# Performance work log

Measured on AMD Instinct MI355X. Metric: run time of the kernel, lower is better.

The kernel has to match this reference:

```python
import jax, jax.numpy as jnp
import numpy as np

N_NODES = 100000
N_EDGES = 50000
NNZ = 800000
D_IN = 128
D_OUT = 128


def setup_inputs() -> dict:
    key = jax.random.key(0)
    k1, k2, k3, k4, k5 = jax.random.split(key, 5)
    x_0 = jax.random.normal(k1, (N_NODES, D_IN), dtype=jnp.float32)
    W = jax.random.normal(k2, (D_OUT, D_IN), dtype=jnp.float32) / np.sqrt(D_IN)
    b = jax.random.normal(k3, (D_OUT,), dtype=jnp.float32) * 0.01
    node_ids = jax.random.randint(k4, (NNZ,), 0, N_NODES, dtype=jnp.int32)
    edge_ids = jax.random.randint(k5, (NNZ,), 0, N_EDGES, dtype=jnp.int32)
    return {"x_0": x_0, "W": W, "b": b, "node_ids": node_ids, "edge_ids": edge_ids}


def reference(x_0, W, b, node_ids, edge_ids):
    # Linear transform (no batchnorm: use_bn=False)
    x = x_0 @ W.T + b  # [n_nodes, out_channels]

    # Step 1: hyperedge aggregation (e_aggr='sum'):  m_{0->1} = B_1^T x, reduce=sum
    m01 = jax.ops.segment_sum(x[node_ids], edge_ids, num_segments=N_EDGES)  # [n_edges, d]

    # Step 2: node aggregation (v_aggr='mean'):  m_{1->0} = B_1 m_{0->1}, reduce=mean
    s = jax.ops.segment_sum(m01[edge_ids], node_ids, num_segments=N_NODES)  # [n_nodes, d]
    cnt = jax.ops.segment_sum(jnp.ones((NNZ,), dtype=x.dtype), node_ids, num_segments=N_NODES)
    m10 = s / jnp.maximum(cnt, 1.0)[:, None]

    # Step 3: SAGE update (residual add)
    return x + m10
```

## Files before the change

### kernel.cpp

```cpp
#include <hip/hip_runtime.h>
#include <hip/hip_bf16.h>

#define NN 100000
#define NE 50000
#define NZ 800000
#define D  128
#define NSEG (NE + NN)
#define FILL_P 4
#define FILL_B 782

typedef __bf16 bf16x8 __attribute__((ext_vector_type(8)));
typedef float f32x4 __attribute__((ext_vector_type(4)));

static __device__ __forceinline__ unsigned short f2bf(float f) {
  union { float f; unsigned u; } v; v.f = f;
  unsigned r = (v.u + 0x7FFFu + ((v.u >> 16) & 1u)) >> 16;
  return (unsigned short)r;
}
static __device__ __forceinline__ float bf2f(unsigned short h) {
  union { unsigned u; float f; } v; v.u = ((unsigned)h) << 16;
  return v.f;
}

__global__ __launch_bounds__(256) void unisage_gemm_mfma(const float* __restrict__ x0,
                                                         const float* __restrict__ W,
                                                         const float* __restrict__ bias,
                                                         unsigned short* __restrict__ xb) {
  __shared__ __bf16 Wl[128][136];
  const int t = threadIdx.x;
#pragma unroll
  for (int i = 0; i < 16; ++i) {
    int idx = i * 1024 + t * 4;
    int dout = idx >> 7;
    int k = idx & 127;
    float4 wv = *(const float4*)(W + idx);
    Wl[dout][k + 0] = (__bf16)wv.x;
    Wl[dout][k + 1] = (__bf16)wv.y;
    Wl[dout][k + 2] = (__bf16)wv.z;
    Wl[dout][k + 3] = (__bf16)wv.w;
  }
  __syncthreads();

  const int wave = t >> 6;
  const int lane = t & 63;
  const int lr = lane & 15;
  const int lg = lane >> 4;
  const int rowbase = blockIdx.x * 128 + wave * 32;

  f32x4 acc[2][8] = {};

#pragma unroll
  for (int ks = 0; ks < 4; ++ks) {
    const int k0 = ks * 32 + lg * 8;
    bf16x8 b[8];
#pragma unroll
    for (int cf = 0; cf < 8; ++cf)
      b[cf] = *(const bf16x8*)&Wl[cf * 16 + lr][k0];
#pragma unroll
    for (int rf = 0; rf < 2; ++rf) {
      int row = rowbase + rf * 16 + lr;
      row = row < NN ? row : NN - 1;
      const float* src = x0 + (size_t)row * D + k0;
      float4 f0 = *(const float4*)(src);
      float4 f1 = *(const float4*)(src + 4);
      bf16x8 a;
      a[0] = (__bf16)f0.x; a[1] = (__bf16)f0.y;
      a[2] = (__bf16)f0.z; a[3] = (__bf16)f0.w;
      a[4] = (__bf16)f1.x; a[5] = (__bf16)f1.y;
      a[6] = (__bf16)f1.z; a[7] = (__bf16)f1.w;
#pragma unroll
      for (int cf = 0; cf < 8; ++cf)
        acc[rf][cf] = __builtin_amdgcn_mfma_f32_16x16x32_bf16(a, b[cf], acc[rf][cf], 0, 0, 0);
    }
  }

#pragma unroll
  for (int cf = 0; cf < 8; ++cf) {
    float bv = bias[cf * 16 + lr];
#pragma unroll
    for (int rf = 0; rf < 2; ++rf) {
#pragma unroll
      for (int r = 0; r < 4; ++r) {
        int row = rowbase + rf * 16 + lg * 4 + r;
        if (row < NN)
          xb[(size_t)row * D + cf * 16 + lr] = f2bf(acc[rf][cf][r] + bv);
      }
    }
  }
}

__global__ void unisage_hist_rank(const int* __restrict__ nid, const int* __restrict__ eid,
                                  int* __restrict__ cnt, unsigned int* __restrict__ rank) {
  int base = (blockIdx.x * 256 + threadIdx.x) * 8;
  if (base >= NZ) return;
  int4 ea = *(const int4*)(eid + base);
  int4 eb = *(const int4*)(eid + base + 4);
  int4 na = *(const int4*)(nid + base);
  int4 nb = *(const int4*)(nid + base + 4);
  int e[8] = {ea.x, ea.y, ea.z, ea.w, eb.x, eb.y, eb.z, eb.w};
  int v[8] = {na.x, na.y, na.z, na.w, nb.x, nb.y, nb.z, nb.w};
  unsigned re[8], rn[8];
#pragma unroll
  for (int j = 0; j < 8; ++j) re[j] = (unsigned)atomicAdd(&cnt[e[j]], 1);
#pragma unroll
  for (int j = 0; j < 8; ++j) rn[j] = (unsigned)atomicAdd(&cnt[NE + v[j]], 1);
  uint4 r0, r1;
  r0.x = (re[0] & 0xffffu) | (rn[0] << 16);
  r0.y = (re[1] & 0xffffu) | (rn[1] << 16);
  r0.z = (re[2] & 0xffffu) | (rn[2] << 16);
  r0.w = (re[3] & 0xffffu) | (rn[3] << 16);
  r1.x = (re[4] & 0xffffu) | (rn[4] << 16);
  r1.y = (re[5] & 0xffffu) | (rn[5] << 16);
  r1.z = (re[6] & 0xffffu) | (rn[6] << 16);
  r1.w = (re[7] & 0xffffu) | (rn[7] << 16);
  *(uint4*)(rank + base) = r0;
  *(uint4*)(rank + base + 4) = r1;
}

__global__ void unisage_scan_k1(const int* __restrict__ in, int* __restrict__ bsum, int n) {
  __shared__ int sh[256];
  int t = threadIdx.x;
  int base = blockIdx.x * 1024 + t * 4;
  int s = 0;
#pragma unroll
  for (int j = 0; j < 4; ++j)
    if (base + j < n) s += in[base + j];
  sh[t] = s;
  __syncthreads();
  for (int o = 128; o > 0; o >>= 1) {
    if (t < o) sh[t] += sh[t + o];
    __syncthreads();
  }
  if (t == 0) bsum[blockIdx.x] = sh[0];
}

__global__ void unisage_scan_k2(const int* __restrict__ bsum, int* __restrict__ bsumx, int nb) {
  __shared__ int sh[256];
  int t = threadIdx.x;
  int v = (t < nb) ? bsum[t] : 0;
  sh[t] = v;
  __syncthreads();
  for (int o = 1; o < 256; o <<= 1) {
    int add = (t >= o) ? sh[t - o] : 0;
    __syncthreads();
    sh[t] += add;
    __syncthreads();
  }
  if (t < nb) bsumx[t] = sh[t] - v;
}

__global__ void unisage_scan_k3(const int* __restrict__ in, const int* __restrict__ bsumx,
                                int* __restrict__ out, int n) {
  __shared__ int sh[256];
  int t = threadIdx.x;
  int base = blockIdx.x * 1024 + t * 4;
  int v[4];
#pragma unroll
  for (int j = 0; j < 4; ++j) v[j] = (base + j < n) ? in[base + j] : 0;
  int tsum = v[0] + v[1] + v[2] + v[3];
  sh[t] = tsum;
  __syncthreads();
  for (int o = 1; o < 256; o <<= 1) {
    int add = (t >= o) ? sh[t - o] : 0;
    __syncthreads();
    sh[t] += add;
    __syncthreads();
  }
  int run = sh[t] - tsum + bsumx[blockIdx.x];
#pragma unroll
  for (int j = 0; j < 4; ++j) {
    if (base + j < n) out[base + j] = run;
    run += v[j];
  }
}

__global__ void unisage_fill(const int* __restrict__ nid, const int* __restrict__ eid,
                             const unsigned int* __restrict__ rank,
                             const int* __restrict__ off,
                             int* __restrict__ csr_e, int* __restrict__ csr_n) {
  const int R = (NSEG + FILL_P - 1) / FILL_P;
  int pass = blockIdx.x / FILL_B;
  int base = ((blockIdx.x % FILL_B) * 256 + threadIdx.x) * 4;
  if (base >= NZ) return;
  int lo = pass * R, hi = lo + R;
  int4 e4 = *(const int4*)(eid + base);
  int4 n4 = *(const int4*)(nid + base);
  uint4 r4 = *(const uint4*)(rank + base);
  int e[4] = {e4.x, e4.y, e4.z, e4.w};
  int v[4] = {n4.x, n4.y, n4.z, n4.w};
  unsigned r[4] = {r4.x, r4.y, r4.z, r4.w};
#pragma unroll
  for (int j = 0; j < 4; ++j) {
    if (e[j] >= lo && e[j] < hi) csr_e[off[e[j]] + (int)(r[j] & 0xffffu)] = v[j];
    int s = NE + v[j];
    if (s >= lo && s < hi) csr_n[off[s] + (int)(r[j] >> 16) - NZ] = e[j];
  }
}

__global__ void unisage_edge_agg(const unsigned short* __restrict__ xb,
                                 const int* __restrict__ csr_e,
                                 const int* __restrict__ off, const int* __restrict__ cnt,
                                 unsigned short* __restrict__ m01b) {
  int w = (blockIdx.x * 256 + threadIdx.x) >> 6;
  int lane = threadIdx.x & 63;
  if (w >= NE) return;
  int beg = off[w];
  int end = beg + cnt[w];
  float ax = 0.f, ay = 0.f;
  for (int base = beg; base < end; base += 64) {
    int m = min(64, end - base);
    int idx = (lane < m) ? csr_e[base + lane] : 0;
    int j = 0;
    for (; j + 3 < m; j += 4) {
      int n0 = __shfl(idx, j, 64);
      int n1 = __shfl(idx, j + 1, 64);
      int n2 = __shfl(idx, j + 2, 64);
      int n3 = __shfl(idx, j + 3, 64);
      ushort2 a = *(const ushort2*)(xb + (size_t)n0 * D + lane * 2);
      ushort2 b = *(const ushort2*)(xb + (size_t)n1 * D + lane * 2);
      ushort2 c = *(const ushort2*)(xb + (size_t)n2 * D + lane * 2);
      ushort2 d = *(const ushort2*)(xb + (size_t)n3 * D + lane * 2);
      ax += (bf2f(a.x) + bf2f(b.x)) + (bf2f(c.x) + bf2f(d.x));
      ay += (bf2f(a.y) + bf2f(b.y)) + (bf2f(c.y) + bf2f(d.y));
    }
    for (; j < m; ++j) {
      int n0 = __shfl(idx, j, 64);
      ushort2 a = *(const ushort2*)(xb + (size_t)n0 * D + lane * 2);
      ax += bf2f(a.x);
      ay += bf2f(a.y);
    }
  }
  ushort2 o; o.x = f2bf(ax); o.y = f2bf(ay);
  *(ushort2*)(m01b + (size_t)w * D + lane * 2) = o;
}

__global__ void unisage_node_agg(const unsigned short* __restrict__ xb,
                                 const unsigned short* __restrict__ m01b,
                                 const int* __restrict__ csr_n,
                                 const int* __restrict__ off, const int* __restrict__ cnt,
                                 float* __restrict__ out) {
  int w = (blockIdx.x * 256 + threadIdx.x) >> 6;
  int lane = threadIdx.x & 63;
  if (w >= NN) return;
  int deg = cnt[NE + w];
  int beg = off[NE + w] - NZ;
  int end = beg + deg;
  float ax = 0.f, ay = 0.f;
  for (int base = beg; base < end; base += 64) {
    int m = min(64, end - base);
    int idx = (lane < m) ? csr_n[base + lane] : 0;
    int j = 0;
    for (; j + 3 < m; j += 4) {
      int e0 = __shfl(idx, j, 64);
      int e1 = __shfl(idx, j + 1, 64);
      int e2 = __shfl(idx, j + 2, 64);
      int e3 = __shfl(idx, j + 3, 64);
      ushort2 a = *(const ushort2*)(m01b + (size_t)e0 * D + lane * 2);
      ushort2 b = *(const ushort2*)(m01b + (size_t)e1 * D + lane * 2);
      ushort2 c = *(const ushort2*)(m01b + (size_t)e2 * D + lane * 2);
      ushort2 d = *(const ushort2*)(m01b + (size_t)e3 * D + lane * 2);
      ax += (bf2f(a.x) + bf2f(b.x)) + (bf2f(c.x) + bf2f(d.x));
      ay += (bf2f(a.y) + bf2f(b.y)) + (bf2f(c.y) + bf2f(d.y));
    }
    for (; j < m; ++j) {
      int e0 = __shfl(idx, j, 64);
      ushort2 a = *(const ushort2*)(m01b + (size_t)e0 * D + lane * 2);
      ax += bf2f(a.x);
      ay += bf2f(a.y);
    }
  }
  float inv = 1.0f / fmaxf((float)deg, 1.0f);
  ushort2 xr = *(const ushort2*)(xb + (size_t)w * D + lane * 2);
  float2 o;
  o.x = bf2f(xr.x) + ax * inv;
  o.y = bf2f(xr.y) + ay * inv;
  *(float2*)(out + (size_t)w * D + lane * 2) = o;
}

extern "C" void kernel_launch(void* const* d_in, const int* in_sizes, int n_in,
                              void* d_out, int out_size, void* d_ws, size_t ws_size,
                              hipStream_t stream) {
  const float* x0   = (const float*)d_in[0];
  const float* W    = (const float*)d_in[1];
  const float* bias = (const float*)d_in[2];
  const int* nid    = (const int*)d_in[3];
  const int* eid    = (const int*)d_in[4];
  float* out = (float*)d_out;

  unsigned short* xb   = (unsigned short*)d_ws;
  unsigned short* m01b = xb + (size_t)NN * D;
  int* cnt   = (int*)(m01b + (size_t)NE * D);
  int* off   = cnt + 150016;
  unsigned int* rank = (unsigned int*)(off + 150016);
  int* csr_e = (int*)(rank + NZ);
  int* csr_n = csr_e + NZ;
  int* bsum  = csr_n + NZ;
  int* bsumx = bsum + 256;

  hipMemsetAsync(cnt, 0, NSEG * sizeof(int), stream);

  unisage_gemm_mfma<<<(NN + 127) / 128, 256, 0, stream>>>(x0, W, bias, xb);

  unisage_hist_rank<<<(NZ / 8 + 255) / 256, 256, 0, stream>>>(nid, eid, cnt, rank);

  const int nb = (NSEG + 1023) / 1024;
  unisage_scan_k1<<<nb, 256, 0, stream>>>(cnt, bsum, NSEG);
  unisage_scan_k2<<<1, 256, 0, stream>>>(bsum, bsumx, nb);
  unisage_scan_k3<<<nb, 256, 0, stream>>>(cnt, bsumx, off, NSEG);

  unisage_fill<<<FILL_P * FILL_B, 256, 0, stream>>>(nid, eid, rank, off, csr_e, csr_n);

  unisage_edge_agg<<<(NE * 64) / 256, 256, 0, stream>>>(xb, csr_e, off, cnt, m01b);
  unisage_node_agg<<<(NN * 64) / 256, 256, 0, stream>>>(xb, m01b, csr_n, off, cnt, out);
}
```

Before: 223.2 us.

## Fuse GEMM with histogram, merge scan stages, widen aggregation gathers

Merges the MFMA linear transform and the edge/node histogram-rank pass into one launch, with blocks split by index. The three-stage scan becomes two: each block of the final stage rescans the block sums itself. Both aggregation kernels now have each 16-lane quarter-wave load a full 256-byte row with 16-byte loads, handling four neighbors per step and combining them with cross-lane xor shuffles. The aim is fewer launches and wider, more parallel gather memory traffic, at the cost of extra shuffle reductions and duplicated scan work.

After: 211.1 us. 5.4% less time.

```diff
diff --git a/kernel.cpp b/kernel.cpp
--- a/kernel.cpp
+++ b/kernel.cpp
@@ -8,6 +8,8 @@
 #define NSEG (NE + NN)
 #define FILL_P 4
 #define FILL_B 782
+#define G_GEMM 782
+#define G_HIST 391
 
 typedef __bf16 bf16x8 __attribute__((ext_vector_type(8)));
 typedef float f32x4 __attribute__((ext_vector_type(4)));
@@ -22,99 +24,102 @@
   return v.f;
 }
 
-__global__ __launch_bounds__(256) void unisage_gemm_mfma(const float* __restrict__ x0,
+__global__ __launch_bounds__(256) void unisage_gemm_hist(const float* __restrict__ x0,
                                                          const float* __restrict__ W,
                                                          const float* __restrict__ bias,
-                                                         unsigned short* __restrict__ xb) {
+                                                         unsigned short* __restrict__ xb,
+                                                         const int* __restrict__ nid,
+                                                         const int* __restrict__ eid,
+                                                         int* __restrict__ cnt,
+                                                         unsigned int* __restrict__ rank) {
   __shared__ __bf16 Wl[128][136];
-  const int t = threadIdx.x;
-#pragma unroll
-  for (int i = 0; i < 16; ++i) {
-    int idx = i * 1024 + t * 4;
-    int dout = idx >> 7;
-    int k = idx & 127;
-    float4 wv = *(const float4*)(W + idx);
-    Wl[dout][k + 0] = (__bf16)wv.x;
-    Wl[dout][k + 1] = (__bf16)wv.y;
-    Wl[dout][k + 2] = (__bf16)wv.z;
-    Wl[dout][k + 3] = (__bf16)wv.w;
-  }
-  __syncthreads();
-
-  const int wave = t >> 6;
-  const int lane = t & 63;
-  const int lr = lane & 15;
-  const int lg = lane >> 4;
-  const int rowbase = blockIdx.x * 128 + wave * 32;
-
-  f32x4 acc[2][8] = {};
-
-#pragma unroll
-  for (int ks = 0; ks < 4; ++ks) {
-    const int k0 = ks * 32 + lg * 8;
-    bf16x8 b[8];
-#pragma unroll
-    for (int cf = 0; cf < 8; ++cf)
-      b[cf] = *(const bf16x8*)&Wl[cf * 16 + lr][k0];
-#pragma unroll
-    for (int rf = 0; rf < 2; ++rf) {
-      int row = rowbase + rf * 16 + lr;
-      row = row < NN ? row : NN - 1;
-      const float* src = x0 + (size_t)row * D + k0;
-      float4 f0 = *(const float4*)(src);
-      float4 f1 = *(const float4*)(src + 4);
-      bf16x8 a;
-      a[0] = (__bf16)f0.x; a[1] = (__bf16)f0.y;
-      a[2] = (__bf16)f0.z; a[3] = (__bf16)f0.w;
-      a[4] = (__bf16)f1.x; a[5] = (__bf16)f1.y;
-      a[6] = (__bf16)f1.z; a[7] = (__bf16)f1.w;
+  if (blockIdx.x < G_GEMM) {
+    const int t = threadIdx.x;
+#pragma unroll
+    for (int i = 0; i < 16; ++i) {
+      int idx = i * 1024 + t * 4;
+      int dout = idx >> 7;
+      int k = idx & 127;
+      float4 wv = *(const float4*)(W + idx);
+      Wl[dout][k + 0] = (__bf16)wv.x;
+      Wl[dout][k + 1] = (__bf16)wv.y;
+      Wl[dout][k + 2] = (__bf16)wv.z;
+      Wl[dout][k + 3] = (__bf16)wv.w;
+    }
+    __syncthreads();
+
+    const int wave = t >> 6;
+    const int lane = t & 63;
+    const int lr = lane & 15;
+    const int lg = lane >> 4;
+    const int rowbase = blockIdx.x * 128 + wave * 32;
+
+    f32x4 acc[2][8] = {};
+
+#pragma unroll
+    for (int ks = 0; ks < 4; ++ks) {
+      const int k0 = ks * 32 + lg * 8;
+      bf16x8 b[8];
 #pragma unroll
       for (int cf = 0; cf < 8; ++cf)
-        acc[rf][cf] = __builtin_amdgcn_mfma_f32_16x16x32_bf16(a, b[cf], acc[rf][cf], 0, 0, 0);
-    }
-  }
-
-#pragma unroll
-  for (int cf = 0; cf < 8; ++cf) {
-    float bv = bias[cf * 16 + lr];
-#pragma unroll
-    for (int rf = 0; rf < 2; ++rf) {
-#pragma unroll
-      for (int r = 0; r < 4; ++r) {
-        int row = rowbase + rf * 16 + lg * 4 + r;
-        if (row < NN)
-          xb[(size_t)row * D + cf * 16 + lr] = f2bf(acc[rf][cf][r] + bv);
+        b[cf] = *(const bf16x8*)&Wl[cf * 16 + lr][k0];
+#pragma unroll
+      for (int rf = 0; rf < 2; ++rf) {
+        int row = rowbase + rf * 16 + lr;
+        row = row < NN ? row : NN - 1;
+        const float* src = x0 + (size_t)row * D + k0;
+        float4 f0 = *(const float4*)(src);
+        float4 f1 = *(const float4*)(src + 4);
+        bf16x8 a;
+        a[0] = (__bf16)f0.x; a[1] = (__bf16)f0.y;
+        a[2] = (__bf16)f0.z; a[3] = (__bf16)f0.w;
+        a[4] = (__bf16)f1.x; a[5] = (__bf16)f1.y;
+        a[6] = (__bf16)f1.z; a[7] = (__bf16)f1.w;
+#pragma unroll
+        for (int cf = 0; cf < 8; ++cf)
+          acc[rf][cf] = __builtin_amdgcn_mfma_f32_16x16x32_bf16(a, b[cf], acc[rf][cf], 0, 0, 0);
       }
     }
-  }
-}
-
-__global__ void unisage_hist_rank(const int* __restrict__ nid, const int* __restrict__ eid,
-                                  int* __restrict__ cnt, unsigned int* __restrict__ rank) {
-  int base = (blockIdx.x * 256 + threadIdx.x) * 8;
-  if (base >= NZ) return;
-  int4 ea = *(const int4*)(eid + base);
-  int4 eb = *(const int4*)(eid + base + 4);
-  int4 na = *(const int4*)(nid + base);
-  int4 nb = *(const int4*)(nid + base + 4);
-  int e[8] = {ea.x, ea.y, ea.z, ea.w, eb.x, eb.y, eb.z, eb.w};
-  int v[8] = {na.x, na.y, na.z, na.w, nb.x, nb.y, nb.z, nb.w};
-  unsigned re[8], rn[8];
-#pragma unroll
-  for (int j = 0; j < 8; ++j) re[j] = (unsigned)atomicAdd(&cnt[e[j]], 1);
-#pragma unroll
-  for (int j = 0; j < 8; ++j) rn[j] = (unsigned)atomicAdd(&cnt[NE + v[j]], 1);
-  uint4 r0, r1;
-  r0.x = (re[0] & 0xffffu) | (rn[0] << 16);
-  r0.y = (re[1] & 0xffffu) | (rn[1] << 16);
-  r0.z = (re[2] & 0xffffu) | (rn[2] << 16);
-  r0.w = (re[3] & 0xffffu) | (rn[3] << 16);
-  r1.x = (re[4] & 0xffffu) | (rn[4] << 16);
-  r1.y = (re[5] & 0xffffu) | (rn[5] << 16);
-  r1.z = (re[6] & 0xffffu) | (rn[6] << 16);
-  r1.w = (re[7] & 0xffffu) | (rn[7] << 16);
-  *(uint4*)(rank + base) = r0;
-  *(uint4*)(rank + base + 4) = r1;
+
+#pragma unroll
+    for (int cf = 0; cf < 8; ++cf) {
+      float bv = bias[cf * 16 + lr];
+#pragma unroll
+      for (int rf = 0; rf < 2; ++rf) {
+#pragma unroll
+        for (int r = 0; r < 4; ++r) {
+          int row = rowbase + rf * 16 + lg * 4 + r;
+          if (row < NN)
+            xb[(size_t)row * D + cf * 16 + lr] = f2bf(acc[rf][cf][r] + bv);
+        }
+      }
+    }
+  } else {
+    int base = ((blockIdx.x - G_GEMM) * 256 + threadIdx.x) * 8;
+    if (base >= NZ) return;
+    int4 ea = *(const int4*)(eid + base);
+    int4 eb = *(const int4*)(eid + base + 4);
+    int4 na = *(const int4*)(nid + base);
+    int4 nb = *(const int4*)(nid + base + 4);
+    int e[8] = {ea.x, ea.y, ea.z, ea.w, eb.x, eb.y, eb.z, eb.w};
+    int v[8] = {na.x, na.y, na.z, na.w, nb.x, nb.y, nb.z, nb.w};
+    unsigned re[8], rn[8];
+#pragma unroll
+    for (int j = 0; j < 8; ++j) re[j] = (unsigned)atomicAdd(&cnt[e[j]], 1);
+#pragma unroll
+    for (int j = 0; j < 8; ++j) rn[j] = (unsigned)atomicAdd(&cnt[NE + v[j]], 1);
+    uint4 r0, r1;
+    r0.x = (re[0] & 0xffffu) | (rn[0] << 16);
+    r0.y = (re[1] & 0xffffu) | (rn[1] << 16);
+    r0.z = (re[2] & 0xffffu) | (rn[2] << 16);
+    r0.w = (re[3] & 0xffffu) | (rn[3] << 16);
+    r1.x = (re[4] & 0xffffu) | (rn[4] << 16);
+    r1.y = (re[5] & 0xffffu) | (rn[5] << 16);
+    r1.z = (re[6] & 0xffffu) | (rn[6] << 16);
+    r1.w = (re[7] & 0xffffu) | (rn[7] << 16);
+    *(uint4*)(rank + base) = r0;
+    *(uint4*)(rank + base + 4) = r1;
+  }
 }
 
 __global__ void unisage_scan_k1(const int* __restrict__ in, int* __restrict__ bsum, int n) {
@@ -134,11 +139,12 @@
   if (t == 0) bsum[blockIdx.x] = sh[0];
 }
 
-__global__ void unisage_scan_k2(const int* __restrict__ bsum, int* __restrict__ bsumx, int nb) {
+__global__ void unisage_scan_k3(const int* __restrict__ in, const int* __restrict__ bsum,
+                                int* __restrict__ out, int n, int nb) {
   __shared__ int sh[256];
   int t = threadIdx.x;
-  int v = (t < nb) ? bsum[t] : 0;
-  sh[t] = v;
+  int bv = (t < nb) ? bsum[t] : 0;
+  sh[t] = bv;
   __syncthreads();
   for (int o = 1; o < 256; o <<= 1) {
     int add = (t >= o) ? sh[t - o] : 0;
@@ -146,13 +152,9 @@
     sh[t] += add;
     __syncthreads();
   }
-  if (t < nb) bsumx[t] = sh[t] - v;
-}
-
-__global__ void unisage_scan_k3(const int* __restrict__ in, const int* __restrict__ bsumx,
-                                int* __restrict__ out, int n) {
-  __shared__ int sh[256];
-  int t = threadIdx.x;
+  int bbase = (blockIdx.x == 0) ? 0 : sh[blockIdx.x - 1];
+  __syncthreads();
+
   int base = blockIdx.x * 1024 + t * 4;
   int v[4];
 #pragma unroll
@@ -166,7 +168,7 @@
     sh[t] += add;
     __syncthreads();
   }
-  int run = sh[t] - tsum + bsumx[blockIdx.x];
+  int run = sh[t] - tsum + bbase;
 #pragma unroll
   for (int j = 0; j < 4; ++j) {
     if (base + j < n) out[base + j] = run;
@@ -197,6 +199,8 @@
   }
 }
 
+#define QRED(x) { x += __shfl_xor(x, 16, 64); x += __shfl_xor(x, 32, 64); }
+
 __global__ void unisage_edge_agg(const unsigned short* __restrict__ xb,
                                  const int* __restrict__ csr_e,
                                  const int* __restrict__ off, const int* __restrict__ cnt,
@@ -204,34 +208,37 @@
   int w = (blockIdx.x * 256 + threadIdx.x) >> 6;
   int lane = threadIdx.x & 63;
   if (w >= NE) return;
+  int quad = lane >> 4;
+  int sl = lane & 15;
   int beg = off[w];
-  int end = beg + cnt[w];
-  float ax = 0.f, ay = 0.f;
+  int deg = cnt[w];
+  int end = beg + deg;
+  float a0 = 0, a1 = 0, a2 = 0, a3 = 0, a4 = 0, a5 = 0, a6 = 0, a7 = 0;
   for (int base = beg; base < end; base += 64) {
     int m = min(64, end - base);
     int idx = (lane < m) ? csr_e[base + lane] : 0;
-    int j = 0;
-    for (; j + 3 < m; j += 4) {
-      int n0 = __shfl(idx, j, 64);
-      int n1 = __shfl(idx, j + 1, 64);
-      int n2 = __shfl(idx, j + 2, 64);
-      int n3 = __shfl(idx, j + 3, 64);
-      ushort2 a = *(const ushort2*)(xb + (size_t)n0 * D + lane * 2);
-      ushort2 b = *(const ushort2*)(xb + (size_t)n1 * D + lane * 2);
-      ushort2 c = *(const ushort2*)(xb + (size_t)n2 * D + lane * 2);
-      ushort2 d = *(const ushort2*)(xb + (size_t)n3 * D + lane * 2);
-      ax += (bf2f(a.x) + bf2f(b.x)) + (bf2f(c.x) + bf2f(d.x));
-      ay += (bf2f(a.y) + bf2f(b.y)) + (bf2f(c.y) + bf2f(d.y));
-    }
-    for (; j < m; ++j) {
-      int n0 = __shfl(idx, j, 64);
-      ushort2 a = *(const ushort2*)(xb + (size_t)n0 * D + lane * 2);
-      ax += bf2f(a.x);
-      ay += bf2f(a.y);
-    }
-  }
-  ushort2 o; o.x = f2bf(ax); o.y = f2bf(ay);
-  *(ushort2*)(m01b + (size_t)w * D + lane * 2) = o;
+    int iters = (m + 3) >> 2;
+    for (int jj = 0; jj < iters; ++jj) {
+      int p = 4 * jj + quad;
+      int r = __shfl(idx, p, 64);
+      if (p < m) {
+        uint4 vv = *(const uint4*)(xb + (size_t)r * D + sl * 8);
+        a0 += bf2f((unsigned short)(vv.x & 0xffffu)); a1 += bf2f((unsigned short)(vv.x >> 16));
+        a2 += bf2f((unsigned short)(vv.y & 0xffffu)); a3 += bf2f((unsigned short)(vv.y >> 16));
+        a4 += bf2f((unsigned short)(vv.z & 0xffffu)); a5 += bf2f((unsigned short)(vv.z >> 16));
+        a6 += bf2f((unsigned short)(vv.w & 0xffffu)); a7 += bf2f((unsigned short)(vv.w >> 16));
+      }
+    }
+  }
+  QRED(a0) QRED(a1) QRED(a2) QRED(a3) QRED(a4) QRED(a5) QRED(a6) QRED(a7)
+  if (quad == 0) {
+    uint4 o;
+    o.x = (unsigned)f2bf(a0) | ((unsigned)f2bf(a1) << 16);
+    o.y = (unsigned)f2bf(a2) | ((unsigned)f2bf(a3) << 16);
+    o.z = (unsigned)f2bf(a4) | ((unsigned)f2bf(a5) << 16);
+    o.w = (unsigned)f2bf(a6) | ((unsigned)f2bf(a7) << 16);
+    *(uint4*)(m01b + (size_t)w * D + sl * 8) = o;
+  }
 }
 
 __global__ void unisage_node_agg(const unsigned short* __restrict__ xb,
@@ -242,39 +249,44 @@
   int w = (blockIdx.x * 256 + threadIdx.x) >> 6;
   int lane = threadIdx.x & 63;
   if (w >= NN) return;
+  int quad = lane >> 4;
+  int sl = lane & 15;
   int deg = cnt[NE + w];
   int beg = off[NE + w] - NZ;
   int end = beg + deg;
-  float ax = 0.f, ay = 0.f;
+  float a0 = 0, a1 = 0, a2 = 0, a3 = 0, a4 = 0, a5 = 0, a6 = 0, a7 = 0;
   for (int base = beg; base < end; base += 64) {
     int m = min(64, end - base);
     int idx = (lane < m) ? csr_n[base + lane] : 0;
-    int j = 0;
-    for (; j + 3 < m; j += 4) {
-      int e0 = __shfl(idx, j, 64);
-      int e1 = __shfl(idx, j + 1, 64);
-      int e2 = __shfl(idx, j + 2, 64);
-      int e3 = __shfl(idx, j + 3, 64);
-      ushort2 a = *(const ushort2*)(m01b + (size_t)e0 * D + lane * 2);
-      ushort2 b = *(const ushort2*)(m01b + (size_t)e1 * D + lane * 2);
-      ushort2 c = *(const ushort2*)(m01b + (size_t)e2 * D + lane * 2);
-      ushort2 d = *(const ushort2*)(m01b + (size_t)e3 * D + lane * 2);
-      ax += (bf2f(a.x) + bf2f(b.x)) + (bf2f(c.x) + bf2f(d.x));
-      ay += (bf2f(a.y) + bf2f(b.y)) + (bf2f(c.y) + bf2f(d.y));
-    }
-    for (; j < m; ++j) {
-      int e0 = __shfl(idx, j, 64);
-      ushort2 a = *(const ushort2*)(m01b + (size_t)e0 * D + lane * 2);
-      ax += bf2f(a.x);
-      ay += bf2f(a.y);
-    }
-  }
-  float inv = 1.0f / fmaxf((float)deg, 1.0f);
-  ushort2 xr = *(const ushort2*)(xb + (size_t)w * D + lane * 2);
-  float2 o;
-  o.x = bf2f(xr.x) + ax * inv;
-  o.y = bf2f(xr.y) + ay * inv;
-  *(float2*)(out + (size_t)w * D + lane * 2) = o;
+    int iters = (m + 3) >> 2;
+    for (int jj = 0; jj < iters; ++jj) {
+      int p = 4 * jj + quad;
+      int r = __shfl(idx, p, 64);
+      if (p < m) {
+        uint4 vv = *(const uint4*)(m01b + (size_t)r * D + sl * 8);
+        a0 += bf2f((unsigned short)(vv.x & 0xffffu)); a1 += bf2f((unsigned short)(vv.x >> 16));
+        a2 += bf2f((unsigned short)(vv.y & 0xffffu)); a3 += bf2f((unsigned short)(vv.y >> 16));
+        a4 += bf2f((unsigned short)(vv.z & 0xffffu)); a5 += bf2f((unsigned short)(vv.z >> 16));
+        a6 += bf2f((unsigned short)(vv.w & 0xffffu)); a7 += bf2f((unsigned short)(vv.w >> 16));
+      }
+    }
+  }
+  QRED(a0) QRED(a1) QRED(a2) QRED(a3) QRED(a4) QRED(a5) QRED(a6) QRED(a7)
+  if (quad == 0) {
+    float inv = 1.0f / fmaxf((float)deg, 1.0f);
+    uint4 xr = *(const uint4*)(xb + (size_t)w * D + sl * 8);
+    float4 o0, o1;
+    o0.x = bf2f((unsigned short)(xr.x & 0xffffu)) + a0 * inv;
+    o0.y = bf2f((unsigned short)(xr.x >> 16))     + a1 * inv;
+    o0.z = bf2f((unsigned short)(xr.y & 0xffffu)) + a2 * inv;
+    o0.w = bf2f((unsigned short)(xr.y >> 16))     + a3 * inv;
+    o1.x = bf2f((unsigned short)(xr.z & 0xffffu)) + a4 * inv;
+    o1.y = bf2f((unsigned short)(xr.z >> 16))     + a5 * inv;
+    o1.z = bf2f((unsigned short)(xr.w & 0xffffu)) + a6 * inv;
+    o1.w = bf2f((unsigned short)(xr.w >> 16))     + a7 * inv;
+    *(float4*)(out + (size_t)w * D + sl * 8) = o0;
+    *(float4*)(out + (size_t)w * D + sl * 8 + 4) = o1;
+  }
 }
 
 extern "C" void kernel_launch(void* const* d_in, const int* in_sizes, int n_in,
@@ -295,18 +307,14 @@
   int* csr_e = (int*)(rank + NZ);
   int* csr_n = csr_e + NZ;
   int* bsum  = csr_n + NZ;
-  int* bsumx = bsum + 256;
 
   hipMemsetAsync(cnt, 0, NSEG * sizeof(int), stream);
 
-  unisage_gemm_mfma<<<(NN + 127) / 128, 256, 0, stream>>>(x0, W, bias, xb);
-
-  unisage_hist_rank<<<(NZ / 8 + 255) / 256, 256, 0, stream>>>(nid, eid, cnt, rank);
+  unisage_gemm_hist<<<G_GEMM + G_HIST, 256, 0, stream>>>(x0, W, bias, xb, nid, eid, cnt, rank);
 
   const int nb = (NSEG + 1023) / 1024;
   unisage_scan_k1<<<nb, 256, 0, stream>>>(cnt, bsum, NSEG);
-  unisage_scan_k2<<<1, 256, 0, stream>>>(bsum, bsumx, nb);
-  unisage_scan_k3<<<nb, 256, 0, stream>>>(cnt, bsumx, off, NSEG);
+  unisage_scan_k3<<<nb, 256, 0, stream>>>(cnt, bsum, off, NSEG, nb);
 
   unisage_fill<<<FILL_P * FILL_B, 256, 0, stream>>>(nid, eid, rank, off, csr_e, csr_n);
 
```
